# Kernel tuning notes

Measured on AMD Instinct MI355X. Metric: run time of the kernel, lower is better.

## Reference

```python
import jax, jax.numpy as jnp
import numpy as np

N = 4096      # nodes
D = 256       # input_dim
OUT = 256     # output_dim
K = 4         # num_kernels
TOPK = 16
CHEB_T = 2
ROW_TEMP = 1.0
EPS = 1e-9


def setup_inputs() -> dict:
    key = jax.random.key(0)
    ks = jax.random.split(key, 6)
    X = jax.random.normal(ks[0], (N, D), dtype=jnp.float32)
    L_k = jax.random.normal(ks[1], (K, D, D), dtype=jnp.float32) * 0.02
    alpha = jnp.ones((K,), dtype=jnp.float32)
    theta = jax.random.normal(ks[2], (CHEB_T + 1, D), dtype=jnp.float32) * 0.02
    rho_raw = jnp.zeros((), dtype=jnp.float32)
    proj_w = jax.random.normal(ks[3], (OUT, D), dtype=jnp.float32) / np.float32(np.sqrt(D))
    proj_b = jnp.zeros((OUT,), dtype=jnp.float32)
    v0 = jax.random.normal(ks[4], (N, 1), dtype=jnp.float32)  # power-iteration init
    return dict(X=X, L_k=L_k, alpha=alpha, theta=theta, rho_raw=rho_raw,
                proj_w=proj_w, proj_b=proj_b, v0=v0)


def reference(X, L_k, alpha, theta, rho_raw, proj_w, proj_b, v0):
    n, d = X.shape
    k = L_k.shape[0]
    # 1) kernel stack: A_k = X L_k X^T / sqrt(D), row softmax  -> (K,N,N)
    A = jnp.einsum('nd,kde,me->knm', X, L_k, X) / jnp.sqrt(jnp.float32(d))
    H_stack = jax.nn.softmax(A / max(ROW_TEMP, 1e-6), axis=-1)
    w = jax.nn.softmax(alpha)[:, None, None]
    H_fused = (H_stack * w).sum(0)                               # (N,N)
    # 2) soft incidence via per-row top-k + renormalize, scattered into B (N, K*N)
    vals, idx = jax.lax.top_k(H_stack, TOPK)                     # (K,N,TOPK)
    vals = vals / (vals.sum(-1, keepdims=True) + EPS)
    E = k * n
    cols = jnp.arange(k)[:, None, None] * n + jnp.arange(n)[None, :, None]
    cols = jnp.broadcast_to(cols, idx.shape)
    B = jnp.zeros((n, E), X.dtype).at[idx.reshape(-1), cols.reshape(-1)].set(vals.reshape(-1))
    W = jnp.ones((E,), X.dtype)
    # 3) hypergraph Laplacian L = I - Dv^{-1/2} B W De^{-1} B^T Dv^{-1/2}
    De = B.sum(0) + EPS
    Dv = (B * W[None, :]).sum(1) + EPS
    Dv_is = 1.0 / jnp.sqrt(Dv)
    S = (B * (W / De)[None, :]) @ B.T                            # (N,N)
    S_norm = Dv_is[:, None] * S * Dv_is[None, :]
    L = jnp.eye(n, dtype=X.dtype) - S_norm
    # 4) lambda_max via power iteration on detached L (constant, as in torch)
    Ld = jax.lax.stop_gradient(L)
    v = v0 / (jnp.linalg.norm(v0) + EPS)
    for _ in range(5):
        v = Ld @ v
        v = v / (jnp.linalg.norm(v) + EPS)
    lam = jnp.maximum((v.T @ (Ld @ v)).squeeze(), jnp.float32(1e-3))
    lam = jax.lax.stop_gradient(lam)
    # Chebyshev filter
    L_tilde = (2.0 / lam) * L - jnp.eye(n, dtype=X.dtype)
    out = X * theta[0][None, :]
    T0 = X
    T1 = L_tilde @ X
    out = out + T1 * theta[1][None, :]
    for t in range(2, CHEB_T + 1):
        T2 = 2.0 * (L_tilde @ T1) - T0
        out = out + T2 * theta[t][None, :]
        T0, T1 = T1, T2
    Z_spec = jax.nn.elu(out)
    # 5) residual blend with kernel diffusion
    Z_kern = H_fused @ X
    rho = jax.nn.sigmoid(rho_raw)
    Z_mix = rho * Z_spec + (1.0 - rho) * Z_kern
    # 6) final projection
    return Z_mix @ proj_w.T + proj_b[None, :]
```

## Files before the change

kernel.cpp:

```cpp
#include <hip/hip_runtime.h>
#include <math.h>

#define N_ 4096
#define D_ 256
#define K_ 4
#define TK_ 16
#define E_ (K_ * N_)
#define NENT_ (E_ * TK_)

typedef unsigned short u16;
typedef unsigned int u32;
typedef __attribute__((ext_vector_type(8))) short bf16x8;
typedef __attribute__((ext_vector_type(4))) float f32x4;

__device__ __forceinline__ u16 bf16_rne(float x) {
  u32 u = __float_as_uint(x);
  u32 r = u + 0x7FFFu + ((u >> 16) & 1u);
  return (u16)(r >> 16);
}


__global__ void scalars_kernel(const float* __restrict__ alpha,
                               const float* __restrict__ rho_raw,
                               float* __restrict__ scal) {
  if (threadIdx.x == 0) {
    float m = alpha[0];
    for (int k = 1; k < K_; ++k) m = fmaxf(m, alpha[k]);
    float e[K_]; float s = 0.f;
    for (int k = 0; k < K_; ++k) { e[k] = expf(alpha[k] - m); s += e[k]; }
    for (int k = 0; k < K_; ++k) scal[k] = e[k] / s;
    scal[4] = 1.0f / (1.0f + expf(-rho_raw[0]));
  }
}

__global__ void dvis_kernel(const float* __restrict__ DvAcc, float* __restrict__ Dvis) {
  int i = blockIdx.x * 256 + threadIdx.x;
  Dvis[i] = 1.0f / sqrtf(DvAcc[i] + 1e-9f);
}

__global__ void ew_scale(const float* __restrict__ M, const float* __restrict__ Dvis,
                         float* __restrict__ U) {
  int i = blockIdx.x * 256 + threadIdx.x;
  U[i] = Dvis[i >> 8] * M[i];
}

__global__ void cvt_split4(const float* __restrict__ in, u16* __restrict__ hi,
                           u16* __restrict__ lo) {
  int i = (blockIdx.x * 256 + threadIdx.x) * 4;
  float4 v = *(const float4*)(in + i);
  u16 h0 = bf16_rne(v.x), h1 = bf16_rne(v.y), h2 = bf16_rne(v.z), h3 = bf16_rne(v.w);
  float f0 = __uint_as_float((u32)h0 << 16), f1 = __uint_as_float((u32)h1 << 16);
  float f2 = __uint_as_float((u32)h2 << 16), f3 = __uint_as_float((u32)h3 << 16);
  u16 l0 = bf16_rne(v.x - f0), l1 = bf16_rne(v.y - f1);
  u16 l2 = bf16_rne(v.z - f2), l3 = bf16_rne(v.w - f3);
  *(uint2*)(hi + i) = make_uint2((u32)h0 | ((u32)h1 << 16), (u32)h2 | ((u32)h3 << 16));
  *(uint2*)(lo + i) = make_uint2((u32)l0 | ((u32)l1 << 16), (u32)l2 | ((u32)l3 << 16));
}

__global__ __launch_bounds__(256) void transpose_split(const float* __restrict__ X,
                                                       u16* __restrict__ ht,
                                                       u16* __restrict__ lt) {
  __shared__ float tile[32][33];
  const int tx = threadIdx.x & 31, ty = threadIdx.x >> 5;
  const int d0 = blockIdx.x * 32, n0 = blockIdx.y * 32;
#pragma unroll
  for (int q = 0; q < 4; ++q)
    tile[ty + q * 8][tx] = X[(size_t)(n0 + ty + q * 8) * D_ + d0 + tx];
  __syncthreads();
#pragma unroll
  for (int q = 0; q < 4; ++q) {
    int dd = ty + q * 8;
    float v = tile[tx][dd];
    u16 h = bf16_rne(v);
    float hf = __uint_as_float((u32)h << 16);
    u16 l = bf16_rne(v - hf);
    ht[(size_t)(d0 + dd) * N_ + n0 + tx] = h;
    lt[(size_t)(d0 + dd) * N_ + n0 + tx] = l;
  }
}

__global__ __launch_bounds__(256) void gemm_nn64_split(const float* __restrict__ A,
                                                       const float* __restrict__ B,
                                                       u16* __restrict__ Ch,
                                                       u16* __restrict__ Cl,
                                                       int Kdim, int lda, int ldb, int ldc) {
  __shared__ float As[16][68];
  __shared__ float Bs[16][68];
  const int tid = threadIdx.x;
  const int bm = blockIdx.x * 64, bn = blockIdx.y * 64;
  const int lrA = tid >> 2, lcA = (tid & 3) * 4;
  const int rrB = tid >> 4, ccB = (tid & 15) * 4;
  const int tx = tid & 15, ty = tid >> 4;
  const float* Ap = A + (size_t)(bm + lrA) * lda + lcA;
  const float* Bp = B + (size_t)rrB * ldb + bn + ccB;
  float acc[4][4] = {};
  for (int k0 = 0; k0 < Kdim; k0 += 16) {
    float4 av = *(const float4*)(Ap + k0);
    float4 bv = *(const float4*)(Bp + (size_t)k0 * ldb);
    __syncthreads();
    As[lcA + 0][lrA] = av.x; As[lcA + 1][lrA] = av.y;
    As[lcA + 2][lrA] = av.z; As[lcA + 3][lrA] = av.w;
    *(float4*)&Bs[rrB][ccB] = bv;
    __syncthreads();
#pragma unroll
    for (int kk = 0; kk < 16; ++kk) {
      float a[4], b[4];
      *(float4*)a = *(const float4*)&As[kk][ty * 4];
      *(float4*)b = *(const float4*)&Bs[kk][tx * 4];
#pragma unroll
      for (int i = 0; i < 4; ++i)
#pragma unroll
        for (int j = 0; j < 4; ++j) acc[i][j] += a[i] * b[j];
    }
  }
#pragma unroll
  for (int i = 0; i < 4; ++i) {
    int row = bm + ty * 4 + i;
    u16 h[4], lo[4];
#pragma unroll
    for (int j = 0; j < 4; ++j) {
      h[j] = bf16_rne(acc[i][j]);
      lo[j] = bf16_rne(acc[i][j] - __uint_as_float((u32)h[j] << 16));
    }
    size_t base = (size_t)row * ldc + bn + tx * 4;
    *(uint2*)(Ch + base) = make_uint2((u32)h[0] | ((u32)h[1] << 16), (u32)h[2] | ((u32)h[3] << 16));
    *(uint2*)(Cl + base) = make_uint2((u32)lo[0] | ((u32)lo[1] << 16), (u32)lo[2] | ((u32)lo[3] << 16));
  }
}

__global__ __launch_bounds__(256) void gemm_nt64_bias(const float* __restrict__ A,
                                                      const float* __restrict__ B,
                                                      const float* __restrict__ bias,
                                                      float* __restrict__ C,
                                                      int Kdim, int lda, int ldb, int ldc) {
  __shared__ float As[16][68];
  __shared__ float Bs[16][68];
  const int tid = threadIdx.x;
  const int bm = blockIdx.x * 64, bn = blockIdx.y * 64;
  const int lr = tid >> 2, lc = (tid & 3) * 4;
  const int tx = tid & 15, ty = tid >> 4;
  const float* Ap = A + (size_t)(bm + lr) * lda + lc;
  const float* Bp = B + (size_t)(bn + lr) * ldb + lc;
  float acc[4][4] = {};
  for (int k0 = 0; k0 < Kdim; k0 += 16) {
    float4 av = *(const float4*)(Ap + k0);
    float4 bv = *(const float4*)(Bp + k0);
    __syncthreads();
    As[lc + 0][lr] = av.x; As[lc + 1][lr] = av.y; As[lc + 2][lr] = av.z; As[lc + 3][lr] = av.w;
    Bs[lc + 0][lr] = bv.x; Bs[lc + 1][lr] = bv.y; Bs[lc + 2][lr] = bv.z; Bs[lc + 3][lr] = bv.w;
    __syncthreads();
#pragma unroll
    for (int kk = 0; kk < 16; ++kk) {
      float a[4], b[4];
      *(float4*)a = *(const float4*)&As[kk][ty * 4];
      *(float4*)b = *(const float4*)&Bs[kk][tx * 4];
#pragma unroll
      for (int i = 0; i < 4; ++i)
#pragma unroll
        for (int j = 0; j < 4; ++j) acc[i][j] += a[i] * b[j];
    }
  }
#pragma unroll
  for (int i = 0; i < 4; ++i) {
    int row = bm + ty * 4 + i;
    float4 o;
    o.x = acc[i][0] + bias[bn + tx * 4 + 0];
    o.y = acc[i][1] + bias[bn + tx * 4 + 1];
    o.z = acc[i][2] + bias[bn + tx * 4 + 2];
    o.w = acc[i][3] + bias[bn + tx * 4 + 3];
    *(float4*)(C + (size_t)row * ldc + bn + tx * 4) = o;
  }
}


__global__ __launch_bounds__(256) void scores_mfma(const u16* __restrict__ Ahg,
                                                   const u16* __restrict__ Alg,
                                                   const u16* __restrict__ Bhg,
                                                   const u16* __restrict__ Blg,
                                                   float* __restrict__ C, float scale) {
  __shared__ char smem[65536];
  const int tid = threadIdx.x;
  const int bm = blockIdx.x * 128, bn = blockIdx.y * 128;
  const int w = tid >> 6, l = tid & 63;
  const int wr = (w >> 1) * 64, wc = (w & 1) * 64;
  const int srow = tid >> 3, scol = (tid & 7) * 8;
  const int lb = l & 15, lke = (l >> 4) * 8;
  const u16* bh0 = Bhg + (size_t)(bn + wc + 0  + lb) * D_ + lke;
  const u16* bh1 = Bhg + (size_t)(bn + wc + 16 + lb) * D_ + lke;
  const u16* bh2 = Bhg + (size_t)(bn + wc + 32 + lb) * D_ + lke;
  const u16* bh3 = Bhg + (size_t)(bn + wc + 48 + lb) * D_ + lke;
  const size_t dlo = (size_t)(Blg - Bhg);
  const int aoff[4] = {
    (srow + 0)  * 128 + ((scol * 2) ^ (((srow + 0)  & 7) << 4)),
    (srow + 32) * 128 + ((scol * 2) ^ (((srow + 32) & 7) << 4)),
    (srow + 64) * 128 + ((scol * 2) ^ (((srow + 64) & 7) << 4)),
    (srow + 96) * 128 + ((scol * 2) ^ (((srow + 96) & 7) << 4)) };
  f32x4 acc[4][4];
#pragma unroll
  for (int i = 0; i < 4; ++i)
#pragma unroll
    for (int j = 0; j < 4; ++j) { acc[i][j][0] = 0.f; acc[i][j][1] = 0.f; acc[i][j][2] = 0.f; acc[i][j][3] = 0.f; }

  uint4 ah[4], al[4];
#pragma unroll
  for (int ii = 0; ii < 4; ++ii) {
    int r = srow + ii * 32;
    ah[ii] = *(const uint4*)(Ahg + (size_t)(bm + r) * D_ + scol);
    al[ii] = *(const uint4*)(Alg + (size_t)(bm + r) * D_ + scol);
  }
  {
    char* bAh = smem; char* bAl = smem + 16384;
#pragma unroll
    for (int ii = 0; ii < 4; ++ii) {
      *(uint4*)(bAh + aoff[ii]) = ah[ii];
      *(uint4*)(bAl + aoff[ii]) = al[ii];
    }
  }
  __syncthreads();

  for (int c = 0; c < 4; ++c) {
    char* bAh = smem + ((c & 1) << 15);
    char* bAl = bAh + 16384;
    const bool hn = (c < 3);
    if (hn) {
      const int kn = (c + 1) * 64;
#pragma unroll
      for (int ii = 0; ii < 4; ++ii) {
        int r = srow + ii * 32;
        ah[ii] = *(const uint4*)(Ahg + (size_t)(bm + r) * D_ + kn + scol);
        al[ii] = *(const uint4*)(Alg + (size_t)(bm + r) * D_ + kn + scol);
      }
    }
#pragma unroll
    for (int kk = 0; kk < 2; ++kk) {
      const int kb = kk * 64 + ((l >> 4) << 4);
      const int ge = c * 64 + kk * 32;
      bf16x8 fbh[4], fbl[4];
      fbh[0] = *(const bf16x8*)(bh0 + ge); fbl[0] = *(const bf16x8*)(bh0 + dlo + ge);
      fbh[1] = *(const bf16x8*)(bh1 + ge); fbl[1] = *(const bf16x8*)(bh1 + dlo + ge);
      fbh[2] = *(const bf16x8*)(bh2 + ge); fbl[2] = *(const bf16x8*)(bh2 + dlo + ge);
      fbh[3] = *(const bf16x8*)(bh3 + ge); fbl[3] = *(const bf16x8*)(bh3 + dlo + ge);
#pragma unroll
      for (int i = 0; i < 4; ++i) {
        int ra = wr + i * 16 + lb;
        int oa = ra * 128 + (kb ^ ((ra & 7) << 4));
        bf16x8 fah = *(const bf16x8*)(bAh + oa);
        bf16x8 fal = *(const bf16x8*)(bAl + oa);
#pragma unroll
        for (int j = 0; j < 4; ++j) {
          acc[i][j] = __builtin_amdgcn_mfma_f32_16x16x32_bf16(fah, fbh[j], acc[i][j], 0, 0, 0);
          acc[i][j] = __builtin_amdgcn_mfma_f32_16x16x32_bf16(fah, fbl[j], acc[i][j], 0, 0, 0);
          acc[i][j] = __builtin_amdgcn_mfma_f32_16x16x32_bf16(fal, fbh[j], acc[i][j], 0, 0, 0);
        }
      }
    }
    if (hn) {
      char* nAh = smem + (((c + 1) & 1) << 15);
      char* nAl = nAh + 16384;
#pragma unroll
      for (int ii = 0; ii < 4; ++ii) {
        *(uint4*)(nAh + aoff[ii]) = ah[ii];
        *(uint4*)(nAl + aoff[ii]) = al[ii];
      }
    }
    __syncthreads();
  }
  float* Cs = (float*)smem;
  const int cr = (l >> 4) * 4, cc = l & 15;
#pragma unroll
  for (int p = 0; p < 2; ++p) {
    __syncthreads();
    if ((w >> 1) == p) {
#pragma unroll
      for (int i = 0; i < 4; ++i)
#pragma unroll
        for (int r = 0; r < 4; ++r) {
          int rl = i * 16 + cr + r;
          int sw = ((rl >> 2) & 3) << 4;
#pragma unroll
          for (int j = 0; j < 4; ++j) {
            int cl = wc + j * 16 + cc;
            Cs[rl * 128 + (cl ^ sw)] = acc[i][j][r] * scale;
          }
        }
    }
    __syncthreads();
#pragma unroll
    for (int ii = 0; ii < 8; ++ii) {
      int rl = ii * 8 + (tid >> 5);
      int c4 = (tid & 31) * 4;
      float4 v = *(float4*)&Cs[rl * 128 + (c4 ^ (((rl >> 2) & 3) << 4))];
      *(float4*)(C + (size_t)(bm + p * 64 + rl) * N_ + bn + c4) = v;
    }
  }
}

__global__ __launch_bounds__(256) void zkern_mfma(const float* __restrict__ S,
                                                  const float* __restrict__ rowmax,
                                                  const float* __restrict__ rowZ,
                                                  const u16* __restrict__ BhT,
                                                  const u16* __restrict__ BlT,
                                                  float* __restrict__ Zpart,
                                                  const float* __restrict__ scal,
                                                  int kidx, int kchunk) {
  __shared__ char smem[65536];
  const int tid = threadIdx.x;
  const int bm = blockIdx.x * 128, bn = blockIdx.y * 128;
  const int kz = blockIdx.z;
  const int w = tid >> 6, l = tid & 63;
  const int wr = (w >> 1) * 64, wc = (w & 1) * 64;
  const int arow = tid >> 4, acol = (tid & 15) * 4;
  const int lb = l & 15, lke = (l >> 4) * 8;
  const u16* bh0 = BhT + (size_t)(bn + wc + 0  + lb) * N_ + lke;
  const u16* bh1 = BhT + (size_t)(bn + wc + 16 + lb) * N_ + lke;
  const u16* bh2 = BhT + (size_t)(bn + wc + 32 + lb) * N_ + lke;
  const u16* bh3 = BhT + (size_t)(bn + wc + 48 + lb) * N_ + lke;
  const size_t dlo = (size_t)(BlT - BhT);
  float rm[8];
  int aoff[8];
#pragma unroll
  for (int ii = 0; ii < 8; ++ii) {
    int r = arow + ii * 16;
    rm[ii] = rowmax[bm + r];
    aoff[ii] = r * 128 + ((acol * 2) ^ ((r & 7) << 4));
  }
  f32x4 acc[4][4];
#pragma unroll
  for (int i = 0; i < 4; ++i)
#pragma unroll
    for (int j = 0; j < 4; ++j) { acc[i][j][0] = 0.f; acc[i][j][1] = 0.f; acc[i][j][2] = 0.f; acc[i][j][3] = 0.f; }

  const int nchunk = kchunk >> 6;
  const int kbase = kz * kchunk;

  float4 sv[8];
#pragma unroll
  for (int ii = 0; ii < 8; ++ii)
    sv[ii] = *(const float4*)(S + (size_t)(bm + arow + ii * 16) * N_ + kbase + acol);
  {
    char* bAh = smem; char* bAl = smem + 16384;
#pragma unroll
    for (int ii = 0; ii < 8; ++ii) {
      float e0 = expf(sv[ii].x - rm[ii]), e1 = expf(sv[ii].y - rm[ii]);
      float e2 = expf(sv[ii].z - rm[ii]), e3 = expf(sv[ii].w - rm[ii]);
      u16 h0 = bf16_rne(e0), h1 = bf16_rne(e1), h2 = bf16_rne(e2), h3 = bf16_rne(e3);
      u16 l0 = bf16_rne(e0 - __uint_as_float((u32)h0 << 16));
      u16 l1 = bf16_rne(e1 - __uint_as_float((u32)h1 << 16));
      u16 l2 = bf16_rne(e2 - __uint_as_float((u32)h2 << 16));
      u16 l3 = bf16_rne(e3 - __uint_as_float((u32)h3 << 16));
      *(uint2*)(bAh + aoff[ii]) = make_uint2((u32)h0 | ((u32)h1 << 16), (u32)h2 | ((u32)h3 << 16));
      *(uint2*)(bAl + aoff[ii]) = make_uint2((u32)l0 | ((u32)l1 << 16), (u32)l2 | ((u32)l3 << 16));
    }
  }
  __syncthreads();

  for (int c = 0; c < nchunk; ++c) {
    char* bAh = smem + ((c & 1) << 15);
    char* bAl = bAh + 16384;
    const bool hn = (c + 1 < nchunk);
    if (hn) {
      const int kn = kbase + (c + 1) * 64;
#pragma unroll
      for (int ii = 0; ii < 8; ++ii)
        sv[ii] = *(const float4*)(S + (size_t)(bm + arow + ii * 16) * N_ + kn + acol);
    }
#pragma unroll
    for (int kk = 0; kk < 2; ++kk) {
      const int kb = kk * 64 + ((l >> 4) << 4);
      const int ge = kbase + c * 64 + kk * 32;
      bf16x8 fbh[4], fbl[4];
      fbh[0] = *(const bf16x8*)(bh0 + ge); fbl[0] = *(const bf16x8*)(bh0 + dlo + ge);
      fbh[1] = *(const bf16x8*)(bh1 + ge); fbl[1] = *(const bf16x8*)(bh1 + dlo + ge);
      fbh[2] = *(const bf16x8*)(bh2 + ge); fbl[2] = *(const bf16x8*)(bh2 + dlo + ge);
      fbh[3] = *(const bf16x8*)(bh3 + ge); fbl[3] = *(const bf16x8*)(bh3 + dlo + ge);
#pragma unroll
      for (int i = 0; i < 4; ++i) {
        int ra = wr + i * 16 + lb;
        int oa = ra * 128 + (kb ^ ((ra & 7) << 4));
        bf16x8 fah = *(const bf16x8*)(bAh + oa);
        bf16x8 fal = *(const bf16x8*)(bAl + oa);
#pragma unroll
        for (int j = 0; j < 4; ++j) {
          acc[i][j] = __builtin_amdgcn_mfma_f32_16x16x32_bf16(fah, fbh[j], acc[i][j], 0, 0, 0);
          acc[i][j] = __builtin_amdgcn_mfma_f32_16x16x32_bf16(fah, fbl[j], acc[i][j], 0, 0, 0);
          acc[i][j] = __builtin_amdgcn_mfma_f32_16x16x32_bf16(fal, fbh[j], acc[i][j], 0, 0, 0);
        }
      }
    }
    if (hn) {
      char* nAh = smem + (((c + 1) & 1) << 15);
      char* nAl = nAh + 16384;
#pragma unroll
      for (int ii = 0; ii < 8; ++ii) {
        float e0 = expf(sv[ii].x - rm[ii]), e1 = expf(sv[ii].y - rm[ii]);
        float e2 = expf(sv[ii].z - rm[ii]), e3 = expf(sv[ii].w - rm[ii]);
        u16 h0 = bf16_rne(e0), h1 = bf16_rne(e1), h2 = bf16_rne(e2), h3 = bf16_rne(e3);
        u16 l0 = bf16_rne(e0 - __uint_as_float((u32)h0 << 16));
        u16 l1 = bf16_rne(e1 - __uint_as_float((u32)h1 << 16));
        u16 l2 = bf16_rne(e2 - __uint_as_float((u32)h2 << 16));
        u16 l3 = bf16_rne(e3 - __uint_as_float((u32)h3 << 16));
        *(uint2*)(nAh + aoff[ii]) = make_uint2((u32)h0 | ((u32)h1 << 16), (u32)h2 | ((u32)h3 << 16));
        *(uint2*)(nAl + aoff[ii]) = make_uint2((u32)l0 | ((u32)l1 << 16), (u32)l2 | ((u32)l3 << 16));
      }
    }
    __syncthreads();
  }
  const float wk = scal[kidx];
  float* Zp = Zpart + (size_t)kz * N_ * D_;
  float* Cs = (float*)smem;
  const int cr = (l >> 4) * 4, cc = l & 15;
#pragma unroll
  for (int p = 0; p < 2; ++p) {
    __syncthreads();
    if ((w >> 1) == p) {
#pragma unroll
      for (int i = 0; i < 4; ++i)
#pragma unroll
        for (int r = 0; r < 4; ++r) {
          int rl = i * 16 + cr + r;
          int sw = ((rl >> 2) & 3) << 4;
#pragma unroll
          for (int j = 0; j < 4; ++j) {
            int cl = wc + j * 16 + cc;
            Cs[rl * 128 + (cl ^ sw)] = acc[i][j][r];
          }
        }
    }
    __syncthreads();
#pragma unroll
    for (int ii = 0; ii < 8; ++ii) {
      int rl = ii * 8 + (tid >> 5);
      int c4 = (tid & 31) * 4;
      int row = bm + p * 64 + rl;
      float sc = wk / rowZ[row];
      float4 v = *(float4*)&Cs[rl * 128 + (c4 ^ (((rl >> 2) & 3) << 4))];
      float* zb = Zp + (size_t)row * D_ + bn + c4;
      float4 z = *(float4*)zb;
      z.x += sc * v.x; z.y += sc * v.y; z.z += sc * v.z; z.w += sc * v.w;
      *(float4*)zb = z;
    }
  }
}

__global__ __launch_bounds__(256) void rowstats_topk(const float* __restrict__ S,
                                                     float* __restrict__ rowmax,
                                                     float* __restrict__ rowZ,
                                                     float* __restrict__ tkv,
                                                     int* __restrict__ tki) {
  const int row = blockIdx.x, tid = threadIdx.x;
  const int wid = tid >> 6, lane = tid & 63;
  __shared__ int hist[1024];
  __shared__ int P[256];
  __shared__ float cval[256];
  __shared__ int cgi[256];
  __shared__ int ccnt;
  __shared__ int binlo_s;
  __shared__ float rv[4];
  __shared__ float stk[TK_];
  __shared__ int itk[TK_];
  __shared__ float tv16[TK_];
  __shared__ float mzs[3];

  hist[tid] = 0; hist[tid + 256] = 0; hist[tid + 512] = 0; hist[tid + 768] = 0;
  if (tid == 0) ccnt = 0;

  const float4* Sp = (const float4*)(S + (size_t)row * N_);
  float r[16];
  float lmax = -3.4e38f;
#pragma unroll
  for (int it = 0; it < 4; ++it) {
    float4 v = Sp[tid + it * 256];
    r[it * 4 + 0] = v.x; r[it * 4 + 1] = v.y; r[it * 4 + 2] = v.z; r[it * 4 + 3] = v.w;
    lmax = fmaxf(lmax, fmaxf(fmaxf(v.x, v.y), fmaxf(v.z, v.w)));
  }
#pragma unroll
  for (int off = 32; off; off >>= 1) lmax = fmaxf(lmax, __shfl_xor(lmax, off));
  if (lane == 0) rv[wid] = lmax;
  __syncthreads();
  if (tid == 0) mzs[0] = fmaxf(fmaxf(rv[0], rv[1]), fmaxf(rv[2], rv[3]));
  __syncthreads();
  const float M = mzs[0];
  float ls = 0.f;
#pragma unroll
  for (int j = 0; j < 16; ++j) ls += expf(r[j] - M);
#pragma unroll
  for (int off = 32; off; off >>= 1) ls += __shfl_xor(ls, off);
  if (lane == 0) rv[wid] = ls;
  __syncthreads();
  if (tid == 0) {
    float z = rv[0] + rv[1] + rv[2] + rv[3];
    mzs[1] = z; rowmax[row] = M; rowZ[row] = z;
  }
  __syncthreads();
  const float Z = mzs[1];

#pragma unroll
  for (int j = 0; j < 16; ++j) {
    u32 u = __float_as_uint(r[j]);
    u32 key = (u >> 31) ? ~u : (u | 0x80000000u);
    atomicAdd(&hist[key >> 22], 1);
  }
  __syncthreads();
  const int b0 = tid * 4;
  const int h0 = hist[b0], h1 = hist[b0 + 1], h2 = hist[b0 + 2], h3 = hist[b0 + 3];
  P[tid] = h0 + h1 + h2 + h3;
  __syncthreads();
  for (int o = 1; o < 256; o <<= 1) {
    int v = P[tid] + ((tid + o < 256) ? P[tid + o] : 0);
    __syncthreads();
    P[tid] = v;
    __syncthreads();
  }
  {
    int above = (tid < 255) ? P[tid + 1] : 0;
    int s3 = above + h3, s2 = s3 + h2, s1 = s2 + h1, s0 = s1 + h0;
    if (s3 >= TK_ && above < TK_) binlo_s = b0 + 3;
    else if (s2 >= TK_ && s3 < TK_) binlo_s = b0 + 2;
    else if (s1 >= TK_ && s2 < TK_) binlo_s = b0 + 1;
    else if (s0 >= TK_ && s1 < TK_) binlo_s = b0;
  }
  __syncthreads();
  const u32 kmin = (u32)binlo_s << 22;
#pragma unroll
  for (int j = 0; j < 16; ++j) {
    u32 u = __float_as_uint(r[j]);
    u32 key = (u >> 31) ? ~u : (u | 0x80000000u);
    if (key >= kmin) {
      int p = atomicAdd(&ccnt, 1);
      if (p < 256) {
        cval[p] = r[j];
        cgi[p] = 4 * tid + ((j >> 2) << 10) + (j & 3);
      }
    }
  }
  __syncthreads();
  const int nc = min(ccnt, 256);
  for (int t = 0; t < TK_; ++t) {
    if (tid < 64) {
      float bv = -3.4e38f; int bg = 0x7fffffff, bp = -1;
      for (int p = tid; p < nc; p += 64) {
        float v = cval[p]; int g = cgi[p];
        if (v > bv || (v == bv && g < bg)) { bv = v; bg = g; bp = p; }
      }
#pragma unroll
      for (int off = 32; off; off >>= 1) {
        float ov = __shfl_xor(bv, off);
        int og = __shfl_xor(bg, off);
        int op = __shfl_xor(bp, off);
        if (ov > bv || (ov == bv && og < bg)) { bv = ov; bg = og; bp = op; }
      }
      if (tid == 0) { stk[t] = bv; itk[t] = bg; cval[bp] = -3.4e38f; }
    }
    __syncthreads();
  }
  if (tid < TK_) tv16[tid] = expf(stk[tid] - M) / Z;
  __syncthreads();
  if (tid == 0) { float s = 0.f; for (int q = 0; q < TK_; ++q) s += tv16[q]; mzs[2] = s + 1e-9f; }
  __syncthreads();
  if (tid < TK_) {
    tkv[(size_t)row * TK_ + tid] = tv16[tid] / mzs[2];
    tki[(size_t)row * TK_ + tid] = itk[tid];
  }
}

__global__ void edge_scan(const float* __restrict__ tkv, const int* __restrict__ tki,
                          float* __restrict__ DvAcc, int* __restrict__ cnt,
                          float* __restrict__ invDe) {
  int e = blockIdx.x * 256 + threadIdx.x;
  float s = 0.f;
#pragma unroll
  for (int q = 0; q < TK_; ++q) s += tkv[(size_t)e * TK_ + q];
  invDe[e] = 1.0f / (s + 1e-9f);
#pragma unroll
  for (int q = 0; q < TK_; ++q) {
    int m = tki[(size_t)e * TK_ + q];
    atomicAdd(&DvAcc[m], tkv[(size_t)e * TK_ + q]);
    atomicAdd(&cnt[m], 1);
  }
}

__global__ __launch_bounds__(1024) void scan_offsets(const int* __restrict__ cnt,
                                                     int* __restrict__ off,
                                                     int* __restrict__ cur) {
  __shared__ int part[1024];
  const int t = threadIdx.x;
  const int b = t * 4;
  int c0 = cnt[b], c1 = cnt[b + 1], c2 = cnt[b + 2], c3 = cnt[b + 3];
  part[t] = c0 + c1 + c2 + c3;
  __syncthreads();
  for (int o = 1; o < 1024; o <<= 1) {
    int v = part[t] + ((t >= o) ? part[t - o] : 0);
    __syncthreads();
    part[t] = v;
    __syncthreads();
  }
  int ex = (t == 0) ? 0 : part[t - 1];
  off[b] = ex; off[b + 1] = ex + c0; off[b + 2] = ex + c0 + c1; off[b + 3] = ex + c0 + c1 + c2;
  cur[b] = off[b]; cur[b + 1] = off[b + 1]; cur[b + 2] = off[b + 2]; cur[b + 3] = off[b + 3];
  if (t == 1023) off[N_] = part[1023];
}

__global__ void edge_fill(const float* __restrict__ tkv, const int* __restrict__ tki,
                          int* __restrict__ cur, int* __restrict__ ince,
                          float* __restrict__ incv) {
  int e = blockIdx.x * 256 + threadIdx.x;
#pragma unroll
  for (int q = 0; q < TK_; ++q) {
    int m = tki[(size_t)e * TK_ + q];
    int pos = atomicAdd(&cur[m], 1);
    ince[pos] = e;
    incv[pos] = tkv[(size_t)e * TK_ + q];
  }
}

__global__ void pi_init(const float* __restrict__ v0, const float* __restrict__ Dvis,
                        float* __restrict__ v, float* __restrict__ u) {
  int i = blockIdx.x * 256 + threadIdx.x;
  float x = v0[i];
  v[i] = x; u[i] = Dvis[i] * x;
}

__global__ void pi_ye(const float* __restrict__ u, const float* __restrict__ tkv,
                      const int* __restrict__ tki, const float* __restrict__ invDe,
                      float* __restrict__ ye) {
  int e = blockIdx.x * 256 + threadIdx.x;
  const float* tv = tkv + (size_t)e * TK_;
  const int* ti = tki + (size_t)e * TK_;
  float a = 0.f;
#pragma unroll
  for (int q = 0; q < TK_; ++q) a += tv[q] * u[ti[q]];
  ye[e] = a * invDe[e];
}

__global__ void pi_step(const float* __restrict__ v, const float* __restrict__ ye,
                        const int* __restrict__ off, const int* __restrict__ ince,
                        const float* __restrict__ incv, const float* __restrict__ Dvis,
                        float* __restrict__ vn, float* __restrict__ un) {
  int m = blockIdx.x * 256 + threadIdx.x;
  float z = 0.f;
  int j0 = off[m], j1 = off[m + 1];
  for (int j = j0; j < j1; ++j) z += incv[j] * ye[ince[j]];
  float wv = v[m] - Dvis[m] * z;
  vn[m] = wv; un[m] = Dvis[m] * wv;
}

__global__ __launch_bounds__(256) void pi_final(const float* __restrict__ v,
                                                const float* __restrict__ ye,
                                                const int* __restrict__ off,
                                                const int* __restrict__ ince,
                                                const float* __restrict__ incv,
                                                const float* __restrict__ Dvis,
                                                float* __restrict__ partial) {
  __shared__ float r1[256], r2[256];
  int m = blockIdx.x * 256 + threadIdx.x;
  float z = 0.f;
  int j0 = off[m], j1 = off[m + 1];
  for (int j = j0; j < j1; ++j) z += incv[j] * ye[ince[j]];
  float wv = v[m] - Dvis[m] * z;
  r1[threadIdx.x] = v[m] * wv;
  r2[threadIdx.x] = v[m] * v[m];
  __syncthreads();
  for (int s = 128; s; s >>= 1) {
    if (threadIdx.x < s) { r1[threadIdx.x] += r1[threadIdx.x + s]; r2[threadIdx.x] += r2[threadIdx.x + s]; }
    __syncthreads();
  }
  if (threadIdx.x == 0) { partial[blockIdx.x * 2] = r1[0]; partial[blockIdx.x * 2 + 1] = r2[0]; }
}

__global__ void pi_lam(const float* __restrict__ partial, float* __restrict__ scal) {
  if (threadIdx.x == 0) {
    float s1 = 0.f, s2 = 0.f;
    for (int b = 0; b < N_ / 256; ++b) { s1 += partial[2 * b]; s2 += partial[2 * b + 1]; }
    scal[5] = fmaxf(s1 / s2, 1e-3f);
  }
}

__global__ __launch_bounds__(256) void ye_mat(const float* __restrict__ U,
                                              const float* __restrict__ tkv,
                                              const int* __restrict__ tki,
                                              const float* __restrict__ invDe,
                                              float* __restrict__ Ye) {
  const int e = blockIdx.x, d = threadIdx.x;
  __shared__ float sv[TK_];
  __shared__ int si[TK_];
  if (d < TK_) { sv[d] = tkv[(size_t)e * TK_ + d]; si[d] = tki[(size_t)e * TK_ + d]; }
  __syncthreads();
  float a = 0.f;
#pragma unroll
  for (int q = 0; q < TK_; ++q) a += sv[q] * U[(size_t)si[q] * D_ + d];
  Ye[(size_t)e * D_ + d] = a * invDe[e];
}

__global__ __launch_bounds__(256) void bgather_combine(const float* __restrict__ Ye,
                                                       const int* __restrict__ off,
                                                       const int* __restrict__ ince,
                                                       const float* __restrict__ incv,
                                                       const float* __restrict__ Dvis,
                                                       const float* __restrict__ Mx,
                                                       const float* __restrict__ G,
                                                       const float* __restrict__ scal,
                                                       float* __restrict__ out, int mode) {
  const int m = blockIdx.x, d = threadIdx.x;
  const int j0 = off[m], j1 = off[m + 1];
  float z = 0.f;
  for (int j = j0; j < j1; ++j) z += incv[j] * Ye[(size_t)ince[j] * D_ + d];
  const float lam = scal[5];
  const float c = 2.0f / lam;
  const size_t idx = (size_t)m * D_ + d;
  const float zz = Dvis[m] * z;
  float r;
  if (mode == 1) r = (c - 1.0f) * Mx[idx] - c * zz;
  else           r = (2.0f * c - 2.0f) * Mx[idx] - 2.0f * c * zz - G[idx];
  out[idx] = r;
}

__global__ void mix_kernel(const float* __restrict__ X, const float* __restrict__ T1,
                           const float* __restrict__ T2, const float* __restrict__ theta,
                           const float* __restrict__ Zpart, int splitk,
                           const float* __restrict__ scal, float* __restrict__ Zmix) {
  const int i = blockIdx.x * 256 + threadIdx.x;
  const int d = i & (D_ - 1);
  float cheb = X[i] * theta[d] + T1[i] * theta[D_ + d] + T2[i] * theta[2 * D_ + d];
  float zs = cheb > 0.f ? cheb : expm1f(cheb);
  float zk = 0.f;
  for (int s = 0; s < splitk; ++s) zk += Zpart[(size_t)s * N_ * D_ + i];
  const float rho = scal[4];
  Zmix[i] = rho * zs + (1.0f - rho) * zk;
}


extern "C" void kernel_launch(void* const* d_in, const int* in_sizes, int n_in,
                              void* d_out, int out_size, void* d_ws, size_t ws_size,
                              hipStream_t stream) {
  const float* X       = (const float*)d_in[0];
  const float* L_k     = (const float*)d_in[1];
  const float* alpha   = (const float*)d_in[2];
  const float* theta   = (const float*)d_in[3];
  const float* rho_raw = (const float*)d_in[4];
  const float* proj_w  = (const float*)d_in[5];
  const float* proj_b  = (const float*)d_in[6];
  const float* v0      = (const float*)d_in[7];
  float* out = (float*)d_out;

  char* w = (char*)d_ws;
  size_t o = 0;
  auto alloc = [&](size_t bytes) -> char* {
    char* p = w + o; o += (bytes + 255) & ~(size_t)255; return p;
  };
  float* S     = (float*)alloc((size_t)N_ * N_ * 4);
  u16*   Xh    = (u16*)  alloc((size_t)N_ * D_ * 2);
  u16*   Xl    = (u16*)  alloc((size_t)N_ * D_ * 2);
  u16*   XhT   = (u16*)  alloc((size_t)D_ * N_ * 2);
  u16*   XlT   = (u16*)  alloc((size_t)D_ * N_ * 2);
  u16*   XLh   = (u16*)  alloc((size_t)N_ * D_ * 2);
  u16*   XLl   = (u16*)  alloc((size_t)N_ * D_ * 2);
  float* rowmax= (float*)alloc(N_ * 4);
  float* rowZ  = (float*)alloc(N_ * 4);
  float* tkv   = (float*)alloc((size_t)NENT_ * 4);
  int*   tki   = (int*)  alloc((size_t)NENT_ * 4);
  float* invDe = (float*)alloc(E_ * 4);
  float* DvAcc = (float*)alloc(N_ * 4);
  float* Dvis  = (float*)alloc(N_ * 4);
  int*   cnt   = (int*)  alloc(N_ * 4);
  int*   off   = (int*)  alloc((N_ + 1) * 4);
  int*   cur   = (int*)  alloc(N_ * 4);
  int*   ince  = (int*)  alloc((size_t)NENT_ * 4);
  float* incv  = (float*)alloc((size_t)NENT_ * 4);
  float* va    = (float*)alloc(N_ * 4);
  float* ua    = (float*)alloc(N_ * 4);
  float* vbuf  = (float*)alloc(N_ * 4);
  float* ubuf  = (float*)alloc(N_ * 4);
  float* yev   = (float*)alloc(E_ * 4);
  float* part  = (float*)alloc((N_ / 256) * 2 * 4);
  float* scal  = (float*)alloc(256);
  int SPLITK = 8;
  while (SPLITK > 1 && o + (size_t)SPLITK * N_ * D_ * 4 > ws_size) SPLITK >>= 1;
  float* Zpart = (float*)alloc((size_t)SPLITK * N_ * D_ * 4);
  const int kchunk = N_ / SPLITK;
  float* U    = S;
  float* Ye   = S + (size_t)N_ * D_;
  float* T1   = Ye + (size_t)E_ * D_;
  float* T2   = T1 + (size_t)N_ * D_;
  float* Zmix = T2 + (size_t)N_ * D_;

  scalars_kernel<<<1, 64, 0, stream>>>(alpha, rho_raw, scal);
  hipMemsetAsync(Zpart, 0, (size_t)SPLITK * N_ * D_ * 4, stream);
  hipMemsetAsync(DvAcc, 0, N_ * 4, stream);
  hipMemsetAsync(cnt, 0, N_ * 4, stream);

  cvt_split4<<<(N_ * D_ / 4) / 256, 256, 0, stream>>>(X, Xh, Xl);
  transpose_split<<<dim3(D_ / 32, N_ / 32), 256, 0, stream>>>(X, XhT, XlT);

  for (int k = 0; k < K_; ++k) {
    gemm_nn64_split<<<dim3(N_ / 64, D_ / 64), 256, 0, stream>>>(
        X, L_k + (size_t)k * D_ * D_, XLh, XLl, D_, D_, D_, D_);
    scores_mfma<<<dim3(N_ / 128, N_ / 128), 256, 0, stream>>>(
        XLh, XLl, Xh, Xl, S, 1.0f / 16.0f);
    rowstats_topk<<<N_, 256, 0, stream>>>(
        S, rowmax, rowZ, tkv + (size_t)k * N_ * TK_, tki + (size_t)k * N_ * TK_);
    zkern_mfma<<<dim3(N_ / 128, D_ / 128, SPLITK), 256, 0, stream>>>(
        S, rowmax, rowZ, XhT, XlT, Zpart, scal, k, kchunk);
  }

  edge_scan<<<E_ / 256, 256, 0, stream>>>(tkv, tki, DvAcc, cnt, invDe);
  dvis_kernel<<<N_ / 256, 256, 0, stream>>>(DvAcc, Dvis);
  scan_offsets<<<1, 1024, 0, stream>>>(cnt, off, cur);
  edge_fill<<<E_ / 256, 256, 0, stream>>>(tkv, tki, cur, ince, incv);

  pi_init<<<N_ / 256, 256, 0, stream>>>(v0, Dvis, va, ua);
  float* vc = va; float* uc = ua; float* vn = vbuf; float* un = ubuf;
  for (int it = 0; it < 5; ++it) {
    pi_ye<<<E_ / 256, 256, 0, stream>>>(uc, tkv, tki, invDe, yev);
    pi_step<<<N_ / 256, 256, 0, stream>>>(vc, yev, off, ince, incv, Dvis, vn, un);
    float* tv = vc; vc = vn; vn = tv;
    float* tu = uc; uc = un; un = tu;
  }
  pi_ye<<<E_ / 256, 256, 0, stream>>>(uc, tkv, tki, invDe, yev);
  pi_final<<<N_ / 256, 256, 0, stream>>>(vc, yev, off, ince, incv, Dvis, part);
  pi_lam<<<1, 64, 0, stream>>>(part, scal);

  ew_scale<<<N_ * D_ / 256, 256, 0, stream>>>(X, Dvis, U);
  ye_mat<<<E_, 256, 0, stream>>>(U, tkv, tki, invDe, Ye);
  bgather_combine<<<N_, 256, 0, stream>>>(Ye, off, ince, incv, Dvis, X, X, scal, T1, 1);
  ew_scale<<<N_ * D_ / 256, 256, 0, stream>>>(T1, Dvis, U);
  ye_mat<<<E_, 256, 0, stream>>>(U, tkv, tki, invDe, Ye);
  bgather_combine<<<N_, 256, 0, stream>>>(Ye, off, ince, incv, Dvis, T1, X, scal, T2, 2);

  mix_kernel<<<N_ * D_ / 256, 256, 0, stream>>>(X, T1, T2, theta, Zpart, SPLITK, scal, Zmix);

  gemm_nt64_bias<<<dim3(N_ / 64, D_ / 64), 256, 0, stream>>>(
      Zmix, proj_w, proj_b, out, D_, D_, D_, D_);
}
```

Baseline: 1.276 ms.

## Drop A-lo term in zkern MFMA, fold Dvis into incidence weights, vectorize gathers

The zkern kernel stops splitting the exponentiated scores into hi/lo bf16 parts. It keeps only the hi part and issues two MFMAs per tile instead of three, which also halves LDS use. Separately, Dvis is folded into a per-entry weight array (tkvd), so the ew_scale passes and the u-vector bookkeeping in power iteration go away. ye_mat and bgather_combine now use one wavefront per row with float4 loads. Precision of the kernel-diffusion term drops to roughly bf16 on the softmax numerators, which may affect accuracy tolerance.

```diff
diff --git a/kernel.cpp b/kernel.cpp
--- a/kernel.cpp
+++ b/kernel.cpp
@@ -38,10 +38,10 @@
   Dvis[i] = 1.0f / sqrtf(DvAcc[i] + 1e-9f);
 }
 
-__global__ void ew_scale(const float* __restrict__ M, const float* __restrict__ Dvis,
-                         float* __restrict__ U) {
+__global__ void make_tkvd(const float* __restrict__ tkv, const int* __restrict__ tki,
+                          const float* __restrict__ Dvis, float* __restrict__ tkvd) {
   int i = blockIdx.x * 256 + threadIdx.x;
-  U[i] = Dvis[i >> 8] * M[i];
+  tkvd[i] = tkv[i] * Dvis[tki[i]];
 }
 
 __global__ void cvt_split4(const float* __restrict__ in, u16* __restrict__ hi,
@@ -303,7 +303,7 @@
                                                   float* __restrict__ Zpart,
                                                   const float* __restrict__ scal,
                                                   int kidx, int kchunk) {
-  __shared__ char smem[65536];
+  __shared__ char smem[32768];
   const int tid = threadIdx.x;
   const int bm = blockIdx.x * 128, bn = blockIdx.y * 128;
   const int kz = blockIdx.z;
@@ -338,25 +338,19 @@
   for (int ii = 0; ii < 8; ++ii)
     sv[ii] = *(const float4*)(S + (size_t)(bm + arow + ii * 16) * N_ + kbase + acol);
   {
-    char* bAh = smem; char* bAl = smem + 16384;
+    char* bAh = smem;
 #pragma unroll
     for (int ii = 0; ii < 8; ++ii) {
       float e0 = expf(sv[ii].x - rm[ii]), e1 = expf(sv[ii].y - rm[ii]);
       float e2 = expf(sv[ii].z - rm[ii]), e3 = expf(sv[ii].w - rm[ii]);
       u16 h0 = bf16_rne(e0), h1 = bf16_rne(e1), h2 = bf16_rne(e2), h3 = bf16_rne(e3);
-      u16 l0 = bf16_rne(e0 - __uint_as_float((u32)h0 << 16));
-      u16 l1 = bf16_rne(e1 - __uint_as_float((u32)h1 << 16));
-      u16 l2 = bf16_rne(e2 - __uint_as_float((u32)h2 << 16));
-      u16 l3 = bf16_rne(e3 - __uint_as_float((u32)h3 << 16));
       *(uint2*)(bAh + aoff[ii]) = make_uint2((u32)h0 | ((u32)h1 << 16), (u32)h2 | ((u32)h3 << 16));
-      *(uint2*)(bAl + aoff[ii]) = make_uint2((u32)l0 | ((u32)l1 << 16), (u32)l2 | ((u32)l3 << 16));
     }
   }
   __syncthreads();
 
   for (int c = 0; c < nchunk; ++c) {
-    char* bAh = smem + ((c & 1) << 15);
-    char* bAl = bAh + 16384;
+    char* bAh = smem + ((c & 1) << 14);
     const bool hn = (c + 1 < nchunk);
     if (hn) {
       const int kn = kbase + (c + 1) * 64;
@@ -378,29 +372,21 @@
         int ra = wr + i * 16 + lb;
         int oa = ra * 128 + (kb ^ ((ra & 7) << 4));
         bf16x8 fah = *(const bf16x8*)(bAh + oa);
-        bf16x8 fal = *(const bf16x8*)(bAl + oa);
 #pragma unroll
         for (int j = 0; j < 4; ++j) {
           acc[i][j] = __builtin_amdgcn_mfma_f32_16x16x32_bf16(fah, fbh[j], acc[i][j], 0, 0, 0);
           acc[i][j] = __builtin_amdgcn_mfma_f32_16x16x32_bf16(fah, fbl[j], acc[i][j], 0, 0, 0);
-          acc[i][j] = __builtin_amdgcn_mfma_f32_16x16x32_bf16(fal, fbh[j], acc[i][j], 0, 0, 0);
         }
       }
     }
     if (hn) {
-      char* nAh = smem + (((c + 1) & 1) << 15);
-      char* nAl = nAh + 16384;
+      char* nAh = smem + (((c + 1) & 1) << 14);
 #pragma unroll
       for (int ii = 0; ii < 8; ++ii) {
         float e0 = expf(sv[ii].x - rm[ii]), e1 = expf(sv[ii].y - rm[ii]);
         float e2 = expf(sv[ii].z - rm[ii]), e3 = expf(sv[ii].w - rm[ii]);
         u16 h0 = bf16_rne(e0), h1 = bf16_rne(e1), h2 = bf16_rne(e2), h3 = bf16_rne(e3);
-        u16 l0 = bf16_rne(e0 - __uint_as_float((u32)h0 << 16));
-        u16 l1 = bf16_rne(e1 - __uint_as_float((u32)h1 << 16));
-        u16 l2 = bf16_rne(e2 - __uint_as_float((u32)h2 << 16));
-        u16 l3 = bf16_rne(e3 - __uint_as_float((u32)h3 << 16));
         *(uint2*)(nAh + aoff[ii]) = make_uint2((u32)h0 | ((u32)h1 << 16), (u32)h2 | ((u32)h3 << 16));
-        *(uint2*)(nAl + aoff[ii]) = make_uint2((u32)l0 | ((u32)l1 << 16), (u32)l2 | ((u32)l3 << 16));
       }
     }
     __syncthreads();
@@ -613,35 +599,27 @@
   }
 }
 
-__global__ void pi_init(const float* __restrict__ v0, const float* __restrict__ Dvis,
-                        float* __restrict__ v, float* __restrict__ u) {
-  int i = blockIdx.x * 256 + threadIdx.x;
-  float x = v0[i];
-  v[i] = x; u[i] = Dvis[i] * x;
-}
-
-__global__ void pi_ye(const float* __restrict__ u, const float* __restrict__ tkv,
+__global__ void pi_ye(const float* __restrict__ v, const float* __restrict__ tkvd,
                       const int* __restrict__ tki, const float* __restrict__ invDe,
                       float* __restrict__ ye) {
   int e = blockIdx.x * 256 + threadIdx.x;
-  const float* tv = tkv + (size_t)e * TK_;
+  const float* tv = tkvd + (size_t)e * TK_;
   const int* ti = tki + (size_t)e * TK_;
   float a = 0.f;
 #pragma unroll
-  for (int q = 0; q < TK_; ++q) a += tv[q] * u[ti[q]];
+  for (int q = 0; q < TK_; ++q) a += tv[q] * v[ti[q]];
   ye[e] = a * invDe[e];
 }
 
 __global__ void pi_step(const float* __restrict__ v, const float* __restrict__ ye,
                         const int* __restrict__ off, const int* __restrict__ ince,
                         const float* __restrict__ incv, const float* __restrict__ Dvis,
-                        float* __restrict__ vn, float* __restrict__ un) {
+                        float* __restrict__ vn) {
   int m = blockIdx.x * 256 + threadIdx.x;
   float z = 0.f;
   int j0 = off[m], j1 = off[m + 1];
   for (int j = j0; j < j1; ++j) z += incv[j] * ye[ince[j]];
-  float wv = v[m] - Dvis[m] * z;
-  vn[m] = wv; un[m] = Dvis[m] * wv;
+  vn[m] = v[m] - Dvis[m] * z;
 }
 
 __global__ __launch_bounds__(256) void pi_final(const float* __restrict__ v,
@@ -675,20 +653,25 @@
   }
 }
 
-__global__ __launch_bounds__(256) void ye_mat(const float* __restrict__ U,
-                                              const float* __restrict__ tkv,
+__global__ __launch_bounds__(256) void ye_mat(const float* __restrict__ M,
+                                              const float* __restrict__ tkvd,
                                               const int* __restrict__ tki,
                                               const float* __restrict__ invDe,
                                               float* __restrict__ Ye) {
-  const int e = blockIdx.x, d = threadIdx.x;
-  __shared__ float sv[TK_];
-  __shared__ int si[TK_];
-  if (d < TK_) { sv[d] = tkv[(size_t)e * TK_ + d]; si[d] = tki[(size_t)e * TK_ + d]; }
-  __syncthreads();
-  float a = 0.f;
-#pragma unroll
-  for (int q = 0; q < TK_; ++q) a += sv[q] * U[(size_t)si[q] * D_ + d];
-  Ye[(size_t)e * D_ + d] = a * invDe[e];
+  const int w = threadIdx.x >> 6, l = threadIdx.x & 63;
+  const int e = blockIdx.x * 4 + w;
+  const float* tv = tkvd + (size_t)e * TK_;
+  const int* ti = tki + (size_t)e * TK_;
+  float4 a = make_float4(0.f, 0.f, 0.f, 0.f);
+#pragma unroll
+  for (int q = 0; q < TK_; ++q) {
+    float v = tv[q];
+    const float4 x = *(const float4*)(M + (size_t)ti[q] * D_ + l * 4);
+    a.x += v * x.x; a.y += v * x.y; a.z += v * x.z; a.w += v * x.w;
+  }
+  const float s = invDe[e];
+  float4 o; o.x = a.x * s; o.y = a.y * s; o.z = a.z * s; o.w = a.w * s;
+  *(float4*)(Ye + (size_t)e * D_ + l * 4) = o;
 }
 
 __global__ __launch_bounds__(256) void bgather_combine(const float* __restrict__ Ye,
@@ -700,18 +683,45 @@
                                                        const float* __restrict__ G,
                                                        const float* __restrict__ scal,
                                                        float* __restrict__ out, int mode) {
-  const int m = blockIdx.x, d = threadIdx.x;
+  const int w = threadIdx.x >> 6, l = threadIdx.x & 63;
+  const int m = blockIdx.x * 4 + w;
   const int j0 = off[m], j1 = off[m + 1];
-  float z = 0.f;
-  for (int j = j0; j < j1; ++j) z += incv[j] * Ye[(size_t)ince[j] * D_ + d];
+  float4 z = make_float4(0.f, 0.f, 0.f, 0.f);
+  int j = j0;
+  for (; j + 2 <= j1; j += 2) {
+    float v0 = incv[j];     int e0 = ince[j];
+    float v1 = incv[j + 1]; int e1 = ince[j + 1];
+    float4 y0 = *(const float4*)(Ye + (size_t)e0 * D_ + l * 4);
+    float4 y1 = *(const float4*)(Ye + (size_t)e1 * D_ + l * 4);
+    z.x += v0 * y0.x + v1 * y1.x;
+    z.y += v0 * y0.y + v1 * y1.y;
+    z.z += v0 * y0.z + v1 * y1.z;
+    z.w += v0 * y0.w + v1 * y1.w;
+  }
+  if (j < j1) {
+    float v0 = incv[j]; int e0 = ince[j];
+    float4 y0 = *(const float4*)(Ye + (size_t)e0 * D_ + l * 4);
+    z.x += v0 * y0.x; z.y += v0 * y0.y; z.z += v0 * y0.z; z.w += v0 * y0.w;
+  }
   const float lam = scal[5];
   const float c = 2.0f / lam;
-  const size_t idx = (size_t)m * D_ + d;
-  const float zz = Dvis[m] * z;
-  float r;
-  if (mode == 1) r = (c - 1.0f) * Mx[idx] - c * zz;
-  else           r = (2.0f * c - 2.0f) * Mx[idx] - 2.0f * c * zz - G[idx];
-  out[idx] = r;
+  const float dv = Dvis[m];
+  const size_t idx = (size_t)m * D_ + l * 4;
+  float4 mx = *(const float4*)(Mx + idx);
+  float4 o;
+  if (mode == 1) {
+    o.x = (c - 1.0f) * mx.x - c * dv * z.x;
+    o.y = (c - 1.0f) * mx.y - c * dv * z.y;
+    o.z = (c - 1.0f) * mx.z - c * dv * z.z;
+    o.w = (c - 1.0f) * mx.w - c * dv * z.w;
+  } else {
+    float4 g = *(const float4*)(G + idx);
+    o.x = (2.0f * c - 2.0f) * mx.x - 2.0f * c * dv * z.x - g.x;
+    o.y = (2.0f * c - 2.0f) * mx.y - 2.0f * c * dv * z.y - g.y;
+    o.z = (2.0f * c - 2.0f) * mx.z - 2.0f * c * dv * z.z - g.z;
+    o.w = (2.0f * c - 2.0f) * mx.w - 2.0f * c * dv * z.w - g.w;
+  }
+  *(float4*)(out + idx) = o;
 }
 
 __global__ void mix_kernel(const float* __restrict__ X, const float* __restrict__ T1,
@@ -758,6 +768,7 @@
   float* rowZ  = (float*)alloc(N_ * 4);
   float* tkv   = (float*)alloc((size_t)NENT_ * 4);
   int*   tki   = (int*)  alloc((size_t)NENT_ * 4);
+  float* tkvd  = (float*)alloc((size_t)NENT_ * 4);
   float* invDe = (float*)alloc(E_ * 4);
   float* DvAcc = (float*)alloc(N_ * 4);
   float* Dvis  = (float*)alloc(N_ * 4);
@@ -767,9 +778,7 @@
   int*   ince  = (int*)  alloc((size_t)NENT_ * 4);
   float* incv  = (float*)alloc((size_t)NENT_ * 4);
   float* va    = (float*)alloc(N_ * 4);
-  float* ua    = (float*)alloc(N_ * 4);
   float* vbuf  = (float*)alloc(N_ * 4);
-  float* ubuf  = (float*)alloc(N_ * 4);
   float* yev   = (float*)alloc(E_ * 4);
   float* part  = (float*)alloc((N_ / 256) * 2 * 4);
   float* scal  = (float*)alloc(256);
@@ -777,7 +786,6 @@
   while (SPLITK > 1 && o + (size_t)SPLITK * N_ * D_ * 4 > ws_size) SPLITK >>= 1;
   float* Zpart = (float*)alloc((size_t)SPLITK * N_ * D_ * 4);
   const int kchunk = N_ / SPLITK;
-  float* U    = S;
   float* Ye   = S + (size_t)N_ * D_;
   float* T1   = Ye + (size_t)E_ * D_;
   float* T2   = T1 + (size_t)N_ * D_;
@@ -804,27 +812,26 @@
 
   edge_scan<<<E_ / 256, 256, 0, stream>>>(tkv, tki, DvAcc, cnt, invDe);
   dvis_kernel<<<N_ / 256, 256, 0, stream>>>(DvAcc, Dvis);
+  make_tkvd<<<NENT_ / 256, 256, 0, stream>>>(tkv, tki, Dvis, tkvd);
   scan_offsets<<<1, 1024, 0, stream>>>(cnt, off, cur);
   edge_fill<<<E_ / 256, 256, 0, stream>>>(tkv, tki, cur, ince, incv);
 
-  pi_init<<<N_ / 256, 256, 0, stream>>>(v0, Dvis, va, ua);
-  float* vc = va; float* uc = ua; float* vn = vbuf; float* un = ubuf;
+  const float* vc = v0;
+  float* vn = va;
   for (int it = 0; it < 5; ++it) {
-    pi_ye<<<E_ / 256, 256, 0, stream>>>(uc, tkv, tki, invDe, yev);
-    pi_step<<<N_ / 256, 256, 0, stream>>>(vc, yev, off, ince, incv, Dvis, vn, un);
-    float* tv = vc; vc = vn; vn = tv;
-    float* tu = uc; uc = un; un = tu;
-  }
-  pi_ye<<<E_ / 256, 256, 0, stream>>>(uc, tkv, tki, invDe, yev);
+    pi_ye<<<E_ / 256, 256, 0, stream>>>(vc, tkvd, tki, invDe, yev);
+    pi_step<<<N_ / 256, 256, 0, stream>>>(vc, yev, off, ince, incv, Dvis, vn);
+    vc = vn;
+    vn = (vc == va) ? vbuf : va;
+  }
+  pi_ye<<<E_ / 256, 256, 0, stream>>>(vc, tkvd, tki, invDe, yev);
   pi_final<<<N_ / 256, 256, 0, stream>>>(vc, yev, off, ince, incv, Dvis, part);
   pi_lam<<<1, 64, 0, stream>>>(part, scal);
 
-  ew_scale<<<N_ * D_ / 256, 256, 0, stream>>>(X, Dvis, U);
-  ye_mat<<<E_, 256, 0, stream>>>(U, tkv, tki, invDe, Ye);
-  bgather_combine<<<N_, 256, 0, stream>>>(Ye, off, ince, incv, Dvis, X, X, scal, T1, 1);
-  ew_scale<<<N_ * D_ / 256, 256, 0, stream>>>(T1, Dvis, U);
-  ye_mat<<<E_, 256, 0, stream>>>(U, tkv, tki, invDe, Ye);
-  bgather_combine<<<N_, 256, 0, stream>>>(Ye, off, ince, incv, Dvis, T1, X, scal, T2, 2);
+  ye_mat<<<E_ / 4, 256, 0, stream>>>(X, tkvd, tki, invDe, Ye);
+  bgather_combine<<<N_ / 4, 256, 0, stream>>>(Ye, off, ince, incv, Dvis, X, X, scal, T1, 1);
+  ye_mat<<<E_ / 4, 256, 0, stream>>>(T1, tkvd, tki, invDe, Ye);
+  bgather_combine<<<N_ / 4, 256, 0, stream>>>(Ye, off, ince, incv, Dvis, T1, X, scal, T2, 2);
 
   mix_kernel<<<N_ * D_ / 256, 256, 0, stream>>>(X, T1, T2, theta, Zpart, SPLITK, scal, Zmix);
 
```

Result: faster. 1.191 ms (-6.7%).
